# Kernel tuning notes

Hardware: AMD Instinct MI355X
Metric: run time of the kernel (lower is better)

## Reference

```python
import jax, jax.numpy as jnp
import numpy as np
jax.config.update("jax_enable_x64", True)

TAPS, DELAY = 5, 3
EPS = 1e-6        # DNN_WPE.eps: power clamp before WPE
WPE_EPS = 1e-10   # wpe_one_iteration eps: inverse-power clamp + diag loading


def _signal_framing(Y, L):
    # Y: (..., T) -> (..., T-L+1, L) sliding frames (as_strided equivalent)
    T = Y.shape[-1]
    idx = jnp.arange(T - L + 1)[:, None] + jnp.arange(L)[None, :]
    return Y[..., idx]


def _wpe_one_iteration(Y, power, taps, delay):
    # Y: (B,F,C,T) complex128, power: (B,F,T) float64
    B, F, C, T = Y.shape
    inv_power = 1.0 / jnp.maximum(power, WPE_EPS)
    Tp = T - delay - taps + 1
    # tap-stacked delayed signal, taps axis reversed: (B,F,C,Tp,taps)
    Psi = _signal_framing(Y, taps)[..., :Tp, :][..., ::-1]
    Psi_n = Psi.conj() * inv_power[:, :, None, delay + taps - 1:, None]
    # covariance R: (B,F,taps*C,taps*C); cross-corr P: (B,F,taps,C_e,C_d)
    R = jnp.einsum("bfdtk,bfetl->bfkdle", Psi_n, Psi).reshape(B, F, taps * C, taps * C)
    P = jnp.einsum("bfdtk,bfet->bfked", Psi_n, Y[..., delay + taps - 1:])
    # v: (B,F,C_e,taps*C_d); conj filter G = inv(R) @ v^T  (X = v @ inv(R)^T)
    v = P.transpose(0, 1, 3, 2, 4).reshape(B, F, C, taps * C)
    eye = jnp.eye(taps * C, dtype=R.dtype)
    tr = jnp.trace(R, axis1=-2, axis2=-1).real[..., None, None] / (taps * C)
    G = jnp.linalg.solve(R + WPE_EPS * tr * eye, v.transpose(0, 1, 3, 2))
    G = G.reshape(B, F, taps, C, C)  # (B,F,tau,d,e) conjugated filter matrix
    # reverb tail: sum over taps of filtered, delayed signal
    tail = jnp.zeros_like(Y)
    for tau in range(taps):  # taps=5, small fixed loop
        s = delay + tau
        contrib = jnp.einsum("bfde,bfdt->bfet", G[:, :, tau], Y[..., : T - s])
        tail = tail.at[..., s:].add(contrib)
    return Y - tail


def setup_inputs() -> dict:
    key = jax.random.key(0)
    k1, k2, k3 = jax.random.split(key, 3)
    B, T, C, F = 4, 512, 8, 257
    data_real = jax.random.normal(k1, (B, T, C, F), dtype=jnp.float32)
    data_imag = jax.random.normal(k2, (B, T, C, F), dtype=jnp.float32)
    ilens = jax.random.randint(k3, (B,), 256, T + 1)
    return {"data_real": data_real, "data_imag": data_imag, "ilens": ilens}


def reference(data_real, data_imag, ilens):
    # (B,T,C,F) -> (B,F,C,T)
    data = (data_real + 1j * data_imag).transpose(0, 3, 2, 1)
    # power averaged over channels, clamped (B,F,T)
    power = jnp.maximum(jnp.mean(data.real ** 2 + data.imag ** 2, axis=-2), EPS)
    enh = _wpe_one_iteration(data.astype(jnp.complex128), power.astype(jnp.float64), TAPS, DELAY)
    enh = enh.astype(jnp.complex64)
    T = enh.shape[-1]
    pad = (jnp.arange(T)[None, :] >= ilens[:, None])[:, None, None, :]  # (B,1,1,T)
    enh = jnp.where(pad, 0.0 + 0.0j, enh)
    enh = enh.transpose(0, 3, 2, 1)  # back to (B,T,C,F)
    return enh.real, enh.imag, power
```

## Files before the change

### kernel.cpp

```cpp
#include <hip/hip_runtime.h>
#include <hip/hip_fp16.h>

#define B_ 4
#define T_ 512
#define C_ 8
#define F_ 257
#define TAPS 5
#define DELAY 3
#define N_ 40
#define NA 48
#define TP 505
#define T0 7
#define BF (B_*F_)
#define BTCF ((size_t)B_*T_*C_*F_)
#define YSH 532
#define YPAD 8
#define AUGSZ 1180
#define ZSD 36

typedef _Float16 half8 __attribute__((ext_vector_type(8)));
typedef float floatx4 __attribute__((ext_vector_type(4)));
typedef uint32_t uint32x4 __attribute__((ext_vector_type(4)));

__device__ inline uint32_t h2mul(uint32_t a, uint32_t b) {
    __half2 r = __hmul2(__builtin_bit_cast(__half2, a), __builtin_bit_cast(__half2, b));
    return __builtin_bit_cast(uint32_t, r);
}
__device__ inline uint32_t packf16(float2 v) {
    __half2 h = __floats2half2_rn(v.x, v.y);
    return __builtin_bit_cast(uint32_t, h);
}
__device__ inline half8 mkfrag(uint32_t a, uint32_t b, uint32_t c, uint32_t d) {
    uint32x4 v = {a, b, c, d};
    return __builtin_bit_cast(half8, v);
}
__device__ inline int rowoff(int i) {
    return i * 49 - ((i * (i - 1)) >> 1);
}

struct Frag { half8 X; half8 Y; };

__device__ inline Frag build2(const uint32_t* p, uint32_t sw0, uint32_t sw1,
                              uint32_t sw2, uint32_t sw3) {
    uint32_t q0 = p[0], q1 = p[1], q2 = p[2], q3 = p[3];
    uint32_t q4 = p[4], q5 = p[5], q6 = p[6], q7 = p[7];
    uint32_t x0 = __builtin_amdgcn_perm(q1, q0, 0x05040100);
    uint32_t y0 = __builtin_amdgcn_perm(q1, q0, 0x07060302);
    uint32_t x1 = __builtin_amdgcn_perm(q3, q2, 0x05040100);
    uint32_t y1 = __builtin_amdgcn_perm(q3, q2, 0x07060302);
    uint32_t x2 = __builtin_amdgcn_perm(q5, q4, 0x05040100);
    uint32_t y2 = __builtin_amdgcn_perm(q5, q4, 0x07060302);
    uint32_t x3 = __builtin_amdgcn_perm(q7, q6, 0x05040100);
    uint32_t y3 = __builtin_amdgcn_perm(q7, q6, 0x07060302);
    Frag f;
    f.X = mkfrag(h2mul(x0, sw0), h2mul(x1, sw1), h2mul(x2, sw2), h2mul(x3, sw3));
    f.Y = mkfrag(h2mul(y0, sw0), h2mul(y1, sw1), h2mul(y2, sw2), h2mul(y3, sw3));
    return f;
}
__device__ inline int zs_off(int j) {
    return (j < N_) ? (j & 7) * YSH + (YPAD + 4 - (j >> 3)) : (j - N_) * YSH + (YPAD + T0);
}

__global__ __launch_bounds__(256) void k_transpose_in(const float* __restrict__ in_re,
                                                      const float* __restrict__ in_im,
                                                      float2* __restrict__ Y) {
    __shared__ float2 tile[32][33];
    int ft = blockIdx.x % 9;
    int tt = blockIdx.x / 9;
    int c = blockIdx.y, b = blockIdx.z;
    int tx = threadIdx.x, ty = threadIdx.y;
    int f = ft * 32 + tx;
#pragma unroll
    for (int i = 0; i < 4; ++i) {
        int t = tt * 32 + ty + i * 8;
        if (f < F_) {
            size_t idx = ((size_t)(b * T_ + t) * C_ + c) * F_ + f;
            tile[ty + i * 8][tx] = make_float2(in_re[idx], in_im[idx]);
        }
    }
    __syncthreads();
    int t2 = tt * 32 + tx;
#pragma unroll
    for (int i = 0; i < 4; ++i) {
        int f2 = ft * 32 + ty + i * 8;
        if (f2 < F_) {
            Y[((size_t)(b * F_ + f2) * C_ + c) * T_ + t2] = tile[tx][ty + i * 8];
        }
    }
}

__global__ __launch_bounds__(256) void k_fused(float2* __restrict__ Y,
                                               float* __restrict__ pow_out) {
    __shared__ uint32_t sYh[C_ * YSH];
    __shared__ __align__(16) float uScr[640];
    __shared__ __align__(16) uint32_t sw_pk[256];
    __shared__ __align__(16) float2 sAugU[AUGSZ];
    float* sPow = uScr;
    float2* sGT = (float2*)uScr;
    int bf = blockIdx.x;
    int tid = threadIdx.x;
    float2* Yp = Y + (size_t)bf * C_ * T_;

    {
        const float4* Yp4 = (const float4*)Yp;
        int t0 = 2 * tid;
        float s0 = 0.f, s1 = 0.f;
#pragma unroll 2
        for (int c = 0; c < C_; ++c) {
            float4 v = Yp4[c * (T_ / 2) + tid];
            uint2 pk = make_uint2(packf16(make_float2(v.x, v.y)),
                                  packf16(make_float2(v.z, v.w)));
            *(uint2*)&sYh[c * YSH + YPAD + t0] = pk;
            s0 += v.x * v.x + v.y * v.y;
            s1 += v.z * v.z + v.w * v.w;
        }
        if (tid < 20) {
            int z = (tid < 8) ? tid : (512 + tid);
#pragma unroll
            for (int c = 0; c < C_; ++c) sYh[c * YSH + z] = 0;
        }
        s0 = fmaxf(s0 * (1.0f / C_), 1e-6f);
        s1 = fmaxf(s1 * (1.0f / C_), 1e-6f);
        ((float2*)(pow_out + (size_t)bf * T_))[tid] = make_float2(s0, s1);
        *(float2*)&sPow[t0] = make_float2(s0, s1);
    }
    __syncthreads();

    {
        int k0 = 2 * tid, k1 = k0 + 1;
        float w0 = (k0 < TP) ? rsqrtf(sPow[k0 + T0]) : 0.f;
        float w1 = (k1 < TP) ? rsqrtf(sPow[k1 + T0]) : 0.f;
        sw_pk[tid] = packf16(make_float2(w0, w1));
    }
    __syncthreads();

    int wv = tid >> 6, ln = tid & 63;
    int kg = ln >> 4;
    if (wv < 3) {
        int r16 = ln & 15;
        int offB = zs_off(wv * 16 + r16);
#pragma unroll 1
        for (int mt = 0; mt < 3; ++mt) {
            int offA = zs_off(mt * 16 + r16);
            floatx4 aRe = {0.f, 0.f, 0.f, 0.f};
            floatx4 aIm = {0.f, 0.f, 0.f, 0.f};
#pragma unroll 2
            for (int ks = 0; ks < 16; ++ks) {
                int kbase = ks * 32 + kg * 8;
                uint32x4 sv = *(const uint32x4*)&sw_pk[kbase >> 1];
                Frag B = build2(&sYh[offB + kbase], sv[0], sv[1], sv[2], sv[3]);
                Frag A = build2(&sYh[offA + kbase], sv[0], sv[1], sv[2], sv[3]);
                half8 nYa = -A.Y;
                aRe = __builtin_amdgcn_mfma_f32_16x16x32_f16(A.X, B.X, aRe, 0, 0, 0);
                aRe = __builtin_amdgcn_mfma_f32_16x16x32_f16(A.Y, B.Y, aRe, 0, 0, 0);
                aIm = __builtin_amdgcn_mfma_f32_16x16x32_f16(A.X, B.Y, aIm, 0, 0, 0);
                aIm = __builtin_amdgcn_mfma_f32_16x16x32_f16(nYa, B.X, aIm, 0, 0, 0);
            }
#pragma unroll
            for (int r = 0; r < 4; ++r) {
                int m = mt * 16 + kg * 4 + r;
                int col = wv * 16 + r16;
                if (m < N_ && col >= m)
                    sAugU[rowoff(m) + col - m] = make_float2(aRe[r], aIm[r]);
            }
        }
    }
    __syncthreads();

    if (tid < 64) {
        float dv = (tid < N_) ? sAugU[rowoff(tid)].x : 0.f;
#pragma unroll
        for (int off = 32; off; off >>= 1) dv += __shfl_xor(dv, off, 64);
        if (tid < N_) sAugU[rowoff(tid)].x += 1e-10f * dv / N_;
    }
    __syncthreads();

    {
        int ri = tid >> 4, ci = tid & 15;
#pragma unroll 1
        for (int p = 0; p < N_ - 1; ++p) {
            int rop = rowoff(p);
            float2 piv = sAugU[rop];
            float dnm = piv.x * piv.x + piv.y * piv.y;
            float pix = piv.x / dnm, piy = -piv.y / dnm;
#pragma unroll 1
            for (int i = p + 1 + ri; i < N_; i += 16) {
                float2 api = sAugU[rop + i - p];
                float mx = api.x * pix + api.y * piy;
                float my = api.x * piy - api.y * pix;
                int roi = rowoff(i) - i;
#pragma unroll 1
                for (int j = i + ci; j < NA; j += 16) {
                    float2 apj = sAugU[rop + j - p];
                    float2 v = sAugU[roi + j];
                    v.x -= mx * apj.x - my * apj.y;
                    v.y -= mx * apj.y + my * apj.x;
                    sAugU[roi + j] = v;
                }
            }
            __syncthreads();
        }
    }
    {
        int bc = tid & 7, br = tid >> 3;
#pragma unroll 1
        for (int p = N_ - 1; p > 0; --p) {
            int rop = rowoff(p);
            float2 piv = sAugU[rop];
            float dnm = piv.x * piv.x + piv.y * piv.y;
            float pix = piv.x / dnm, piy = -piv.y / dnm;
            float2 rhs = sAugU[rop + N_ + bc - p];
            float xr = rhs.x * pix - rhs.y * piy;
            float xi = rhs.x * piy + rhs.y * pix;
#pragma unroll 1
            for (int i = br; i < p; i += 32) {
                int roi = rowoff(i) - i;
                float2 aip = sAugU[roi + p];
                float2 v = sAugU[roi + N_ + bc];
                v.x -= aip.x * xr - aip.y * xi;
                v.y -= aip.x * xi + aip.y * xr;
                sAugU[roi + N_ + bc] = v;
            }
            __syncthreads();
        }
    }
    for (int idx = tid; idx < N_ * C_; idx += 256) {
        int j = idx >> 3;
        int e = idx & 7;
        int roj = rowoff(j);
        float2 piv = sAugU[roj];
        float dnm = piv.x * piv.x + piv.y * piv.y;
        float pix = piv.x / dnm, piy = -piv.y / dnm;
        float2 rhs = sAugU[roj + N_ + e - j];
        int tau = j >> 3, d = j & 7;
        sGT[(e * C_ + d) * TAPS + tau] =
            make_float2(rhs.x * pix - rhs.y * piy, rhs.x * piy + rhs.y * pix);
    }
    __syncthreads();

    uint32_t* zRe = (uint32_t*)sAugU;
    uint32_t* zIm = zRe + 32 * ZSD;
    half8 aFr[2], aFi[2];
    {
        int m = ln & 15;
#pragma unroll
        for (int ks = 0; ks < 2; ++ks) {
            half8 hr = {}, hi = {};
#pragma unroll
            for (int q = 0; q < 8; ++q) {
                int j = ks * 32 + kg * 8 + q;
                float gx = 0.f, gy = 0.f;
                if (m < 8 && j < N_) {
                    float2 g = sGT[(m * C_ + (j & 7)) * TAPS + (j >> 3)];
                    gx = g.x; gy = g.y;
                }
                hr[q] = (_Float16)gx;
                hi[q] = (_Float16)gy;
            }
            aFr[ks] = hr;
            aFi[ks] = hi;
        }
    }
    for (int idx = tid; idx < 2 * 32 * ZSD; idx += 256) zRe[idx] = 0;
    __syncthreads();

#pragma unroll 1
    for (int ch = 0; ch < 16; ++ch) {
        int c0 = ch * 32;
        for (int idx = tid; idx < 640; idx += 256) {
            int jp = idx >> 5, tl = idx & 31;
            int j0 = 2 * jp, j1 = j0 + 1;
            int base = c0 + tl + (YPAD - 3);
            uint32_t y0 = sYh[(j0 & 7) * YSH + base - (j0 >> 3)];
            uint32_t y1 = sYh[(j1 & 7) * YSH + base - (j1 >> 3)];
            zRe[tl * ZSD + jp] = __builtin_amdgcn_perm(y1, y0, 0x05040100);
            zIm[tl * ZSD + jp] = __builtin_amdgcn_perm(y1, y0, 0x07060302);
        }
        __syncthreads();
        if (wv < 2) {
            floatx4 accR = {0.f, 0.f, 0.f, 0.f};
            floatx4 accI = {0.f, 0.f, 0.f, 0.f};
            int trow = wv * 16 + (ln & 15);
#pragma unroll
            for (int ks = 0; ks < 2; ++ks) {
                int o = trow * ZSD + ks * 16 + kg * 4;
                half8 Br = __builtin_bit_cast(half8, *(const uint32x4*)&zRe[o]);
                half8 Bi = __builtin_bit_cast(half8, *(const uint32x4*)&zIm[o]);
                half8 nFi = -aFi[ks];
                accR = __builtin_amdgcn_mfma_f32_16x16x32_f16(aFr[ks], Br, accR, 0, 0, 0);
                accR = __builtin_amdgcn_mfma_f32_16x16x32_f16(nFi, Bi, accR, 0, 0, 0);
                accI = __builtin_amdgcn_mfma_f32_16x16x32_f16(aFr[ks], Bi, accI, 0, 0, 0);
                accI = __builtin_amdgcn_mfma_f32_16x16x32_f16(aFi[ks], Br, accI, 0, 0, 0);
            }
            if (kg < 2) {
                int tg = c0 + trow;
#pragma unroll
                for (int r = 0; r < 4; ++r) {
                    int e = kg * 4 + r;
                    float2 cur = Yp[e * T_ + tg];
                    Yp[e * T_ + tg] = make_float2(cur.x - accR[r], cur.y - accI[r]);
                }
            }
        }
        __syncthreads();
    }
}

__global__ __launch_bounds__(256) void k_transpose_out(const float2* __restrict__ Yenh,
                                                       const int* __restrict__ ilens,
                                                       float* __restrict__ out_re,
                                                       float* __restrict__ out_im) {
    __shared__ float2 tile[32][33];
    int ft = blockIdx.x % 9;
    int tt = blockIdx.x / 9;
    int c = blockIdx.y, b = blockIdx.z;
    int tx = threadIdx.x, ty = threadIdx.y;
    int ilen = ilens[b];
    int t = tt * 32 + tx;
#pragma unroll
    for (int i = 0; i < 4; ++i) {
        int f = ft * 32 + ty + i * 8;
        if (f < F_) tile[tx][ty + i * 8] = Yenh[((size_t)(b * F_ + f) * C_ + c) * T_ + t];
    }
    __syncthreads();
    int f2 = ft * 32 + tx;
#pragma unroll
    for (int i = 0; i < 4; ++i) {
        int t2 = tt * 32 + ty + i * 8;
        if (f2 < F_) {
            float2 v = tile[ty + i * 8][tx];
            if (t2 >= ilen) v = make_float2(0.f, 0.f);
            size_t o = ((size_t)(b * T_ + t2) * C_ + c) * F_ + f2;
            out_re[o] = v.x;
            out_im[o] = v.y;
        }
    }
}

extern "C" void kernel_launch(void* const* d_in, const int* in_sizes, int n_in,
                              void* d_out, int out_size, void* d_ws, size_t ws_size,
                              hipStream_t stream) {
    const float* in_re = (const float*)d_in[0];
    const float* in_im = (const float*)d_in[1];
    const int* ilens = (const int*)d_in[2];

    float* out_re = (float*)d_out;
    float* out_im = out_re + BTCF;
    float* out_pw = out_im + BTCF;

    float2* Y = (float2*)d_ws;

    dim3 tb(32, 8);
    dim3 tg(9 * 16, C_, B_);
    k_transpose_in<<<tg, tb, 0, stream>>>(in_re, in_im, Y);
    k_fused<<<BF, 256, 0, stream>>>(Y, out_pw);
    k_transpose_out<<<tg, tb, 0, stream>>>(Y, ilens, out_re, out_im);
}
```

Before: 208.6 us.

## Fuse input/output transposes into main WPE kernel with XCD-aware block mapping

```diff
diff --git a/kernel.cpp b/kernel.cpp
--- a/kernel.cpp
+++ b/kernel.cpp
@@ -61,35 +61,11 @@
     return (j < N_) ? (j & 7) * YSH + (YPAD + 4 - (j >> 3)) : (j - N_) * YSH + (YPAD + T0);
 }
 
-__global__ __launch_bounds__(256) void k_transpose_in(const float* __restrict__ in_re,
-                                                      const float* __restrict__ in_im,
-                                                      float2* __restrict__ Y) {
-    __shared__ float2 tile[32][33];
-    int ft = blockIdx.x % 9;
-    int tt = blockIdx.x / 9;
-    int c = blockIdx.y, b = blockIdx.z;
-    int tx = threadIdx.x, ty = threadIdx.y;
-    int f = ft * 32 + tx;
-#pragma unroll
-    for (int i = 0; i < 4; ++i) {
-        int t = tt * 32 + ty + i * 8;
-        if (f < F_) {
-            size_t idx = ((size_t)(b * T_ + t) * C_ + c) * F_ + f;
-            tile[ty + i * 8][tx] = make_float2(in_re[idx], in_im[idx]);
-        }
-    }
-    __syncthreads();
-    int t2 = tt * 32 + tx;
-#pragma unroll
-    for (int i = 0; i < 4; ++i) {
-        int f2 = ft * 32 + ty + i * 8;
-        if (f2 < F_) {
-            Y[((size_t)(b * F_ + f2) * C_ + c) * T_ + t2] = tile[tx][ty + i * 8];
-        }
-    }
-}
-
-__global__ __launch_bounds__(256) void k_fused(float2* __restrict__ Y,
+__global__ __launch_bounds__(256) void k_fused(const float* __restrict__ in_re,
+                                               const float* __restrict__ in_im,
+                                               const int* __restrict__ ilens,
+                                               float* __restrict__ out_re,
+                                               float* __restrict__ out_im,
                                                float* __restrict__ pow_out) {
     __shared__ uint32_t sYh[C_ * YSH];
     __shared__ __align__(16) float uScr[640];
@@ -97,22 +73,30 @@
     __shared__ __align__(16) float2 sAugU[AUGSZ];
     float* sPow = uScr;
     float2* sGT = (float2*)uScr;
-    int bf = blockIdx.x;
     int tid = threadIdx.x;
-    float2* Yp = Y + (size_t)bf * C_ * T_;
-
-    {
-        const float4* Yp4 = (const float4*)Yp;
-        int t0 = 2 * tid;
+
+    int bid = blockIdx.x;
+    int xcd = bid & 7, slot = bid >> 3;
+    int w = (xcd < 4) ? xcd * 129 + slot : 516 + (xcd - 4) * 128 + slot;
+    int b = w / F_;
+    int f = w - b * F_;
+    int ilen = ilens[b];
+    const float* pre = in_re + (size_t)b * T_ * C_ * F_ + f;
+    const float* pim = in_im + (size_t)b * T_ * C_ * F_ + f;
+
+    {
+        int t0 = tid, t1 = tid + 256;
         float s0 = 0.f, s1 = 0.f;
 #pragma unroll 2
         for (int c = 0; c < C_; ++c) {
-            float4 v = Yp4[c * (T_ / 2) + tid];
-            uint2 pk = make_uint2(packf16(make_float2(v.x, v.y)),
-                                  packf16(make_float2(v.z, v.w)));
-            *(uint2*)&sYh[c * YSH + YPAD + t0] = pk;
-            s0 += v.x * v.x + v.y * v.y;
-            s1 += v.z * v.z + v.w * v.w;
+            size_t a0 = ((size_t)t0 * C_ + c) * F_;
+            size_t a1 = ((size_t)t1 * C_ + c) * F_;
+            float xr0 = pre[a0], xi0 = pim[a0];
+            float xr1 = pre[a1], xi1 = pim[a1];
+            sYh[c * YSH + YPAD + t0] = packf16(make_float2(xr0, xi0));
+            sYh[c * YSH + YPAD + t1] = packf16(make_float2(xr1, xi1));
+            s0 += xr0 * xr0 + xi0 * xi0;
+            s1 += xr1 * xr1 + xi1 * xi1;
         }
         if (tid < 20) {
             int z = (tid < 8) ? tid : (512 + tid);
@@ -121,8 +105,10 @@
         }
         s0 = fmaxf(s0 * (1.0f / C_), 1e-6f);
         s1 = fmaxf(s1 * (1.0f / C_), 1e-6f);
-        ((float2*)(pow_out + (size_t)bf * T_))[tid] = make_float2(s0, s1);
-        *(float2*)&sPow[t0] = make_float2(s0, s1);
+        pow_out[(size_t)w * T_ + t0] = s0;
+        pow_out[(size_t)w * T_ + t1] = s1;
+        sPow[t0] = s0;
+        sPow[t1] = s1;
     }
     __syncthreads();
 
@@ -294,46 +280,21 @@
             }
             if (kg < 2) {
                 int tg = c0 + trow;
+                bool dead = (tg >= ilen);
 #pragma unroll
                 for (int r = 0; r < 4; ++r) {
                     int e = kg * 4 + r;
-                    float2 cur = Yp[e * T_ + tg];
-                    Yp[e * T_ + tg] = make_float2(cur.x - accR[r], cur.y - accI[r]);
+                    size_t a = ((size_t)tg * C_ + e) * F_;
+                    float ex = pre[a] - accR[r];
+                    float ey = pim[a] - accI[r];
+                    if (dead) { ex = 0.f; ey = 0.f; }
+                    size_t o = (size_t)b * T_ * C_ * F_ + f + a;
+                    out_re[o] = ex;
+                    out_im[o] = ey;
                 }
             }
         }
         __syncthreads();
-    }
-}
-
-__global__ __launch_bounds__(256) void k_transpose_out(const float2* __restrict__ Yenh,
-                                                       const int* __restrict__ ilens,
-                                                       float* __restrict__ out_re,
-                                                       float* __restrict__ out_im) {
-    __shared__ float2 tile[32][33];
-    int ft = blockIdx.x % 9;
-    int tt = blockIdx.x / 9;
-    int c = blockIdx.y, b = blockIdx.z;
-    int tx = threadIdx.x, ty = threadIdx.y;
-    int ilen = ilens[b];
-    int t = tt * 32 + tx;
-#pragma unroll
-    for (int i = 0; i < 4; ++i) {
-        int f = ft * 32 + ty + i * 8;
-        if (f < F_) tile[tx][ty + i * 8] = Yenh[((size_t)(b * F_ + f) * C_ + c) * T_ + t];
-    }
-    __syncthreads();
-    int f2 = ft * 32 + tx;
-#pragma unroll
-    for (int i = 0; i < 4; ++i) {
-        int t2 = tt * 32 + ty + i * 8;
-        if (f2 < F_) {
-            float2 v = tile[ty + i * 8][tx];
-            if (t2 >= ilen) v = make_float2(0.f, 0.f);
-            size_t o = ((size_t)(b * T_ + t2) * C_ + c) * F_ + f2;
-            out_re[o] = v.x;
-            out_im[o] = v.y;
-        }
     }
 }
 
@@ -348,11 +309,5 @@
     float* out_im = out_re + BTCF;
     float* out_pw = out_im + BTCF;
 
-    float2* Y = (float2*)d_ws;
-
-    dim3 tb(32, 8);
-    dim3 tg(9 * 16, C_, B_);
-    k_transpose_in<<<tg, tb, 0, stream>>>(in_re, in_im, Y);
-    k_fused<<<BF, 256, 0, stream>>>(Y, out_pw);
-    k_transpose_out<<<tg, tb, 0, stream>>>(Y, ilens, out_re, out_im);
-}
+    k_fused<<<BF, 256, 0, stream>>>(in_re, in_im, ilens, out_re, out_im, out_pw);
+}
```

Measured after the change: 210.4 us. No clear change (+0.9%).
